# Kernel tuning notes

Measured on AMD Instinct MI355X. Metric: run time of the kernel, lower is better.

The kernel has to match this reference:

```python
import jax, jax.numpy as jnp
import numpy as np

B, CIN, COUT, L, K = 4, 512, 512, 4096, 7
DIL, STR = 1, 1
OUT_LEN = (L - DIL * (K - 1) - 1) // STR + 1  # 4090 ('valid' conv output length)


def setup_inputs() -> dict:
    key = jax.random.key(0)
    k1, k2, k3, k4 = jax.random.split(key, 4)
    x = jax.random.normal(k1, (B, CIN, L), dtype=jnp.float32)
    offsets = jax.random.normal(k2, (B, 1, OUT_LEN, K), dtype=jnp.float32)
    # kaiming_uniform_(a=sqrt(5)) on [COUT, CIN, K] -> U(-1/sqrt(fan_in), 1/sqrt(fan_in))
    fan_in = CIN * K
    bound = 1.0 / np.sqrt(fan_in)
    weight = jax.random.uniform(k3, (COUT, CIN, K), dtype=jnp.float32, minval=-bound, maxval=bound)
    bias = jax.random.uniform(k4, (COUT,), dtype=jnp.float32, minval=-bound, maxval=bound)
    return {"x": x, "offsets": offsets, "weight": weight, "bias": bias}


def _deform_interp(x, offsets, kernel_size, dilation, stride):
    # x: [B, C, L]; offsets: [B, 1, out_len, K] (offset_groups == 1)
    Lx = x.shape[-1]
    dil_pos = (jnp.arange(kernel_size) * dilation).astype(offsets.dtype)       # [K]
    out_len = offsets.shape[-2]
    t0s = (jnp.arange(out_len) * stride).astype(offsets.dtype)[:, None]        # [out_len, 1]
    T = t0s + dil_pos + offsets                                                # [B, 1, out_len, K]
    # constrained: each sample must stay inside its receptive field
    T = jnp.maximum(T, t0s)
    T = jnp.minimum(T, t0s + dil_pos[-1])
    U0 = jnp.clip(jnp.floor(T).astype(jnp.int32), 0, Lx - 2)                   # [B, 1, out_len, K]
    U = jnp.stack([U0, U0 + 1], axis=-1)                                       # [B, 1, out_len, K, 2]
    idx = U[:, 0]                                                              # [B, out_len, K, 2]
    # gather along length, broadcast index over channels
    xg = jax.vmap(lambda xb, ib: xb[:, ib])(x, idx)                            # [B, C, out_len, K, 2]
    # linear-interp weights: max(0, 1 - |U - T|)
    G = jnp.maximum(0.0, 1.0 - jnp.abs(U.astype(T.dtype) - T[..., None]))      # [B, 1, out_len, K, 2]
    return jnp.sum(G * xg, axis=-1)                                            # [B, C, out_len, K]


def reference(x, offsets, weight, bias):
    samp = _deform_interp(x, offsets, K, DIL, STR)                             # [B, C, out_len, K]
    # conv1d(weight, stride=K) on flattened [B, C, out_len*K] == per-position full contraction
    out = jnp.einsum('bcok,dck->bdo', samp, weight) + bias[:, None]            # [B, COUT, out_len]
    return out
```

## Files before the change

### kernel.cpp

```cpp
#include <hip/hip_runtime.h>
#include <hip/hip_bf16.h>
#include <stdint.h>

#define B_      4
#define CIN     512
#define COUT    512
#define L_      4096
#define K_      7
#define OUT_LEN 4090

typedef unsigned short ushort_t;
typedef __attribute__((ext_vector_type(8))) __bf16 bf16x8;
typedef __attribute__((ext_vector_type(4))) float f32x4;

__device__ __forceinline__ uint32_t f2bf(float f) {
    uint32_t u = __float_as_uint(f);
    return (u + 0x7fffu + ((u >> 16) & 1u)) >> 16;
}

__device__ __forceinline__ uint32_t pack2bf(float s0, float s1) {
    __hip_bfloat162 h = __float22bfloat162_rn(make_float2(s0, s1));
    uint32_t r;
    __builtin_memcpy(&r, &h, 4);
    return r;
}

__device__ __forceinline__ uint32_t interp1(uint32_t wl, uint32_t wh, float g0, float g1) {
    const float l0 = __uint_as_float(wl << 16);
    const float l1 = __uint_as_float(wl & 0xffff0000u);
    const float h0 = __uint_as_float(wh << 16);
    const float h1 = __uint_as_float(wh & 0xffff0000u);
    return pack2bf(g0 * l0 + g1 * h0, g0 * l1 + g1 * h1);
}

__device__ __forceinline__ void async16(const void* g, void* l) {
    __builtin_amdgcn_global_load_lds(
        (const __attribute__((address_space(1))) unsigned int*)g,
        (__attribute__((address_space(3))) unsigned int*)l, 16, 0, 0);
}


__global__ __launch_bounds__(256)
void reorder_w2_kernel(const float* __restrict__ w, uint32_t* __restrict__ Wr) {
    const int d   = blockIdx.x;
    const int tid = threadIdx.x;
    __shared__ float wrow[3584];
    const float4* src = (const float4*)(w + (size_t)d * 3584);
    for (int e = tid; e < 896; e += 256) ((float4*)wrow)[e] = src[e];
    __syncthreads();
    const int cc  = tid >> 4;
    const int clp = tid & 15;
    const int pos = (((clp >> 2) ^ ((d >> 1) & 3)) << 2) | (clp & 3);
    #pragma unroll
    for (int k = 0; k < K_; ++k) {
        const float w0 = wrow[tid * 14 + k];
        const float w1 = wrow[tid * 14 + 7 + k];
        Wr[((size_t)(cc * 7 + k) * 512 + d) * 16 + pos] = (f2bf(w1) << 16) | f2bf(w0);
    }
}

__global__ __launch_bounds__(256)
void interp_pack_kernel(const float* __restrict__ x, const float* __restrict__ offs,
                        uint32_t* __restrict__ P) {
    const int obx = blockIdx.x;
    const int cc  = blockIdx.y;
    const int b   = blockIdx.z;
    const int tid = threadIdx.x;
    const int o0  = obx * 128;
    __shared__ __align__(16) uint32_t XT[2176];

    const float* xc = x + ((size_t)b * CIN + cc * 32) * L_ + o0;
    #pragma unroll
    for (int r = 0; r < 3; ++r) {
        const int e = r * 256 + tid;
        if (e < 544) {
            const int cp   = e / 34;
            const int col4 = e - cp * 34;
            const int colb = col4 * 4;
            const float* p0 = xc + (size_t)(2 * cp) * L_ + colb;
            const float* p1 = p0 + L_;
            float4 v0, v1;
            if (o0 + colb + 3 < L_) {
                v0 = *(const float4*)p0;
                v1 = *(const float4*)p1;
            } else {
                float a0 = (o0 + colb + 0 < L_) ? p0[0] : 0.f;
                float a1 = (o0 + colb + 1 < L_) ? p0[1] : 0.f;
                float a2 = (o0 + colb + 2 < L_) ? p0[2] : 0.f;
                float a3 = (o0 + colb + 3 < L_) ? p0[3] : 0.f;
                float b0 = (o0 + colb + 0 < L_) ? p1[0] : 0.f;
                float b1 = (o0 + colb + 1 < L_) ? p1[1] : 0.f;
                float b2 = (o0 + colb + 2 < L_) ? p1[2] : 0.f;
                float b3 = (o0 + colb + 3 < L_) ? p1[3] : 0.f;
                v0 = make_float4(a0, a1, a2, a3);
                v1 = make_float4(b0, b1, b2, b3);
            }
            const float* f0 = (const float*)&v0;
            const float* f1 = (const float*)&v1;
            const int cpg = cp >> 1, hh = cp & 1;
            #pragma unroll
            for (int ii = 0; ii < 4; ++ii) {
                const int col = colb + ii;
                XT[col * 16 + (((cpg ^ (col & 7)) << 1) | hh)] = pack2bf(f0[ii], f1[ii]);
            }
        }
    }
    __syncthreads();

    const int o_loc = tid >> 1;
    const int h     = tid & 1;
    int o = o0 + o_loc; if (o > OUT_LEN - 1) o = OUT_LEN - 1;
    const float t0f = (float)o;
    const int sr = (o_loc >> 1) & 3;
    uint32_t* Pb = P + ((size_t)((b * 16 + cc) * 7) * 32 + obx) * 2048 + o_loc * 16;
    const int c0 = ((2 * h) ^ sr) << 2;
    const int c1 = ((2 * h + 1) ^ sr) << 2;
    #pragma unroll
    for (int k = 0; k < K_; ++k) {
        const float off = offs[((size_t)b * OUT_LEN + o) * K_ + k];
        float T = t0f + (float)k + off;
        T = fmaxf(T, t0f);
        T = fminf(T, t0f + 6.0f);
        int u0 = (int)floorf(T); if (u0 > L_ - 2) u0 = L_ - 2;
        const float g1 = T - (float)u0;
        const float g0 = 1.0f - g1;
        const int ul = u0 - o0;
        const uint32_t* R0 = &XT[ul * 16];
        const uint32_t* R1 = &XT[(ul + 1) * 16];
        const int s0 = ul & 7, s1 = (ul + 1) & 7;
        uint32_t ow[8];
        #pragma unroll
        for (int q = 0; q < 4; ++q) {
            const int pg = h * 4 + q;
            const uint2 lo = *(const uint2*)&R0[(pg ^ s0) << 1];
            const uint2 hi = *(const uint2*)&R1[(pg ^ s1) << 1];
            ow[q * 2 + 0] = interp1(lo.x, hi.x, g0, g1);
            ow[q * 2 + 1] = interp1(lo.y, hi.y, g0, g1);
        }
        uint32_t* Pk = Pb + (size_t)k * 65536;
        *(uint4*)&Pk[c0] = make_uint4(ow[0], ow[1], ow[2], ow[3]);
        *(uint4*)&Pk[c1] = make_uint4(ow[4], ow[5], ow[6], ow[7]);
    }
}

__global__ __launch_bounds__(256, 2)
void gemm_kernel(const ushort_t* __restrict__ Wr, const uint32_t* __restrict__ P,
                 const float* __restrict__ bias, float* __restrict__ out) {
    const int bxi  = blockIdx.x;
    const int o0   = bxi * 128;
    const int d0   = blockIdx.y * 128;
    const int b    = blockIdx.z;
    const int tid  = threadIdx.x;
    const int wv   = tid >> 6;
    const int lane = tid & 63;
    const int m16  = lane & 15;
    const int quad = lane >> 4;
    const int wd   = wv >> 1;
    const int wo   = wv & 1;
    const int sw   = (m16 >> 1) & 3;
    const int chk  = (quad ^ sw) * 8;

    __shared__ __align__(16) ushort_t As0[4096], As1[4096], As2[4096], As3[4096];
    __shared__ __align__(16) ushort_t Bs0[4096], Bs1[4096], Bs2[4096], Bs3[4096];

    const int aoff = (wd * 64 + m16) * 32 + chk;
    const int boff = (wo * 64 + m16) * 32 + chk;

    const ushort_t* Ag = Wr + (size_t)d0 * 32 + (size_t)tid * 8;
    const uint32_t* Bg = P + ((size_t)(b * 112) * 32 + bxi) * 2048 + (size_t)tid * 4;

#define ISSUE(S, ASP, BSP)                                                    \
    { _Pragma("unroll") for (int r_ = 0; r_ < 2; ++r_)                        \
        async16(Ag + (size_t)(S) * 16384 + r_ * 2048,                         \
                (void*)((ASP) + (r_ * 256 + wv * 64) * 8));                   \
      _Pragma("unroll") for (int r_ = 0; r_ < 2; ++r_)                        \
        async16(Bg + (size_t)(S) * 65536 + r_ * 1024,                         \
                (void*)((BSP) + (r_ * 256 + wv * 64) * 8)); }

#define WAITBAR(N)                                                            \
    { asm volatile("s_waitcnt vmcnt(" #N ")" ::: "memory");                   \
      __builtin_amdgcn_s_barrier();                                           \
      __builtin_amdgcn_sched_barrier(0); }

#define SSTEP(ASP, BSP)                                                       \
    {                                                                         \
        bf16x8 af_[4], bf_[4];                                                \
        _Pragma("unroll")                                                     \
        for (int i_ = 0; i_ < 4; ++i_) af_[i_] = *(const bf16x8*)&(ASP)[aoff + i_ * 512]; \
        _Pragma("unroll")                                                     \
        for (int j_ = 0; j_ < 4; ++j_) bf_[j_] = *(const bf16x8*)&(BSP)[boff + j_ * 512]; \
        __builtin_amdgcn_s_setprio(1);                                        \
        _Pragma("unroll")                                                     \
        for (int i_ = 0; i_ < 4; ++i_) {                                      \
            _Pragma("unroll")                                                 \
            for (int j_ = 0; j_ < 4; ++j_)                                    \
                acc[i_][j_] = __builtin_amdgcn_mfma_f32_16x16x32_bf16(        \
                    af_[i_], bf_[j_], acc[i_][j_], 0, 0, 0);                  \
        }                                                                     \
        __builtin_amdgcn_s_setprio(0);                                        \
    }

    f32x4 acc[4][4];
    #pragma unroll
    for (int i = 0; i < 4; ++i) {
        #pragma unroll
        for (int j = 0; j < 4; ++j) acc[i][j] = (f32x4){0.f, 0.f, 0.f, 0.f};
    }

    ISSUE(0, As0, Bs0);
    ISSUE(1, As1, Bs1);

    #pragma unroll 1
    for (int t = 0; t < 108; t += 4) {
        ISSUE(t + 2, As2, Bs2); WAITBAR(8); SSTEP(As0, Bs0);
        ISSUE(t + 3, As3, Bs3); WAITBAR(8); SSTEP(As1, Bs1);
        ISSUE(t + 4, As0, Bs0); WAITBAR(8); SSTEP(As2, Bs2);
        ISSUE(t + 5, As1, Bs1); WAITBAR(8); SSTEP(As3, Bs3);
    }
    ISSUE(110, As2, Bs2); WAITBAR(8); SSTEP(As0, Bs0);
    ISSUE(111, As3, Bs3); WAITBAR(8); SSTEP(As1, Bs1);
    WAITBAR(4); SSTEP(As2, Bs2);
    WAITBAR(0); SSTEP(As3, Bs3);

    #pragma unroll
    for (int i = 0; i < 4; ++i) {
        const int dd = d0 + wd * 64 + i * 16 + quad * 4;
        float bv[4];
        #pragma unroll
        for (int r = 0; r < 4; ++r) bv[r] = bias[dd + r];
        #pragma unroll
        for (int j = 0; j < 4; ++j) {
            const int oo = o0 + wo * 64 + j * 16 + m16;
            if (oo < OUT_LEN) {
                float* op = out + (size_t)b * COUT * OUT_LEN + (size_t)dd * OUT_LEN + oo;
                #pragma unroll
                for (int r = 0; r < 4; ++r)
                    op[(size_t)r * OUT_LEN] = acc[i][j][r] + bv[r];
            }
        }
    }
#undef ISSUE
#undef WAITBAR
#undef SSTEP
}


__global__ __launch_bounds__(256)
void reorder_w1_kernel(const float* __restrict__ w, uint32_t* __restrict__ Wr) {
    const int d   = blockIdx.x;
    const int tid = threadIdx.x;
    __shared__ float wrow[3584];
    const float4* src = (const float4*)(w + (size_t)d * 3584);
    for (int e = tid; e < 896; e += 256) ((float4*)wrow)[e] = src[e];
    __syncthreads();
    const int cc  = tid >> 4;
    const int clp = tid & 15;
    #pragma unroll
    for (int k = 0; k < K_; ++k) {
        const float w0 = wrow[tid * 14 + k];
        const float w1 = wrow[tid * 14 + 7 + k];
        Wr[((size_t)((k * 16 + cc) * 512 + d)) * 16 + clp] = (f2bf(w1) << 16) | f2bf(w0);
    }
}

__global__ __launch_bounds__(256)
void prepack_kernel(const float* __restrict__ x, uint32_t* __restrict__ xpack) {
    const int obx = blockIdx.x;
    const int cc  = blockIdx.y;
    const int b   = blockIdx.z;
    const int tid = threadIdx.x;
    const int o0  = obx * 128;
    __shared__ __align__(16) uint32_t XT[2176];
    const float* xc = x + ((size_t)b * CIN + cc * 32) * L_ + o0;
    #pragma unroll
    for (int r = 0; r < 3; ++r) {
        const int e = r * 256 + tid;
        if (e < 544) {
            const int cp   = e / 34;
            const int col4 = e - cp * 34;
            const int colb = col4 * 4;
            const float* p0 = xc + (size_t)(2 * cp) * L_ + colb;
            const float* p1 = p0 + L_;
            float4 v0, v1;
            if (o0 + colb + 3 < L_) {
                v0 = *(const float4*)p0;
                v1 = *(const float4*)p1;
            } else {
                float a0 = (o0 + colb + 0 < L_) ? p0[0] : 0.f;
                float a1 = (o0 + colb + 1 < L_) ? p0[1] : 0.f;
                float a2 = (o0 + colb + 2 < L_) ? p0[2] : 0.f;
                float a3 = (o0 + colb + 3 < L_) ? p0[3] : 0.f;
                float b0 = (o0 + colb + 0 < L_) ? p1[0] : 0.f;
                float b1 = (o0 + colb + 1 < L_) ? p1[1] : 0.f;
                float b2 = (o0 + colb + 2 < L_) ? p1[2] : 0.f;
                float b3 = (o0 + colb + 3 < L_) ? p1[3] : 0.f;
                v0 = make_float4(a0, a1, a2, a3);
                v1 = make_float4(b0, b1, b2, b3);
            }
            const float* f0 = (const float*)&v0;
            const float* f1 = (const float*)&v1;
            const int cpg = cp >> 1, h = cp & 1;
            #pragma unroll
            for (int ii = 0; ii < 4; ++ii) {
                const int col = colb + ii;
                XT[col * 16 + (((cpg ^ (col & 7)) << 1) | h)] = pack2bf(f0[ii], f1[ii]);
            }
        }
    }
    __syncthreads();
    uint4* dst = (uint4*)xpack + (size_t)((b * 16 + cc) * 32 + obx) * 544;
    const uint4* s4 = (const uint4*)XT;
    #pragma unroll
    for (int r = 0; r < 3; ++r) {
        const int e = r * 256 + tid;
        if (e < 544) dst[e] = s4[e];
    }
}

__global__ __launch_bounds__(256, 2)
void fused_v1_kernel(const float* __restrict__ offs, const ushort_t* __restrict__ Wr,
                     const uint32_t* __restrict__ xpack, const float* __restrict__ bias,
                     float* __restrict__ out) {
    const int bxi  = blockIdx.x;
    const int o0   = bxi * 128;
    const int d0   = blockIdx.y * 128;
    const int b    = blockIdx.z;
    const int tid  = threadIdx.x;
    const int wv   = tid >> 6;
    const int lane = tid & 63;
    const int m16  = lane & 15;
    const int quad = lane >> 4;
    const int ob   = wv * 32;
    const int q2   = quad * 2;

    __shared__ __align__(16) ushort_t As0[4096], As1[4096], As2[4096], As3[4096];
    __shared__ __align__(16) uint32_t XTB0[2304], XTB1[2304];
    __shared__ int    SU[896];
    __shared__ float2 PG[896];

#define ISSUE_A(KK, CC, ASP)                                                      \
    {                                                                             \
        _Pragma("unroll")                                                         \
        for (int r_ = 0; r_ < 2; ++r_) {                                          \
            const int c_ = r_ * 256 + tid;                                        \
            const int row_ = c_ >> 2, pc_ = c_ & 3;                               \
            const ushort_t* g_ = Wr                                               \
                + ((size_t)(((KK) * 16 + (CC)) * 512 + d0 + row_)) * 32 + pc_ * 8;\
            async16(g_, (void*)((ASP) + (r_ * 256 + wv * 64) * 8));               \
        }                                                                         \
    }

#define ISSUE_XTB(CC, XP)                                                         \
    {                                                                             \
        const uint32_t* sp_ = xpack + ((size_t)((b * 16 + (CC)) * 32 + bxi)) * 2176; \
        _Pragma("unroll")                                                         \
        for (int r_ = 0; r_ < 3; ++r_) {                                          \
            const int cb_ = r_ * 256 + wv * 64;                                   \
            if (cb_ < 544) {                                                      \
                const int c_ = r_ * 256 + tid;                                    \
                async16((const void*)(sp_ + (size_t)c_ * 4),                      \
                        (void*)((XP) + (size_t)cb_ * 4));                         \
            }                                                                     \
        }                                                                         \
    }

#define STEP(KK, XP, ASP)                                                         \
    {                                                                             \
        bf16x8 af_[8];                                                            \
        _Pragma("unroll")                                                         \
        for (int i_ = 0; i_ < 8; ++i_)                                            \
            af_[i_] = *(const bf16x8*)&(ASP)[(i_ * 16 + m16) * 32 + quad * 8];    \
        bf16x8 bfr_[2];                                                           \
        _Pragma("unroll")                                                         \
        for (int j_ = 0; j_ < 2; ++j_) {                                          \
            const int row_ = ((KK) << 7) | (ob + j_ * 16 + m16);                  \
            const int u_ = SU[row_];                                              \
            const float2 g_ = PG[row_];                                           \
            const uint32_t* Xr0_ = &(XP)[u_ * 16];                                \
            const uint32_t* Xr1_ = Xr0_ + 16;                                     \
            const int s0_ = u_ & 7, s1_ = (u_ + 1) & 7;                           \
            const uint2 a0_ = *(const uint2*)&Xr0_[((q2     ^ s0_) << 1)];        \
            const uint2 a1_ = *(const uint2*)&Xr0_[(((q2+1) ^ s0_) << 1)];        \
            const uint2 c0_ = *(const uint2*)&Xr1_[((q2     ^ s1_) << 1)];        \
            const uint2 c1_ = *(const uint2*)&Xr1_[(((q2+1) ^ s1_) << 1)];        \
            uint4 rr_;                                                            \
            rr_.x = interp1(a0_.x, c0_.x, g_.x, g_.y);                            \
            rr_.y = interp1(a0_.y, c0_.y, g_.x, g_.y);                            \
            rr_.z = interp1(a1_.x, c1_.x, g_.x, g_.y);                            \
            rr_.w = interp1(a1_.y, c1_.y, g_.x, g_.y);                            \
            __builtin_memcpy(&bfr_[j_], &rr_, 16);                                \
        }                                                                         \
        _Pragma("unroll")                                                         \
        for (int i_ = 0; i_ < 8; ++i_) {                                          \
            _Pragma("unroll")                                                     \
            for (int j_ = 0; j_ < 2; ++j_)                                        \
                acc[i_][j_] = __builtin_amdgcn_mfma_f32_16x16x32_bf16(af_[i_], bfr_[j_], acc[i_][j_], 0, 0, 0); \
        }                                                                         \
    }

#define HALF(CCB, A0_, A1_, A2_, A3_)                                             \
    ISSUE_A(2, (CCB), A2_); ISSUE_A(3, (CCB), A3_); ISSUE_XTB((CCB) + 1, XTB1);   \
    STEP(0, XTB0, A0_); STEP(1, XTB0, A1_); __syncthreads();                      \
    ISSUE_A(4, (CCB), A0_); ISSUE_A(5, (CCB), A1_);                               \
    STEP(2, XTB0, A2_); STEP(3, XTB0, A3_); __syncthreads();                      \
    ISSUE_A(6, (CCB), A2_); ISSUE_A(0, (CCB) + 1, A3_);                           \
    STEP(4, XTB0, A0_); STEP(5, XTB0, A1_); __syncthreads();                      \
    ISSUE_A(1, (CCB) + 1, A0_); ISSUE_A(2, (CCB) + 1, A1_);                       \
    STEP(6, XTB0, A2_); STEP(0, XTB1, A3_); __syncthreads();                      \
    ISSUE_A(3, (CCB) + 1, A2_); ISSUE_A(4, (CCB) + 1, A3_);                       \
    if ((CCB) + 2 < 16) { ISSUE_XTB((CCB) + 2, XTB0); }                           \
    STEP(1, XTB1, A0_); STEP(2, XTB1, A1_); __syncthreads();                      \
    ISSUE_A(5, (CCB) + 1, A0_); ISSUE_A(6, (CCB) + 1, A1_);                       \
    STEP(3, XTB1, A2_); STEP(4, XTB1, A3_); __syncthreads();                      \
    if ((CCB) + 2 < 16) { ISSUE_A(0, (CCB) + 2, A2_); ISSUE_A(1, (CCB) + 2, A3_); } \
    STEP(5, XTB1, A0_); STEP(6, XTB1, A1_); __syncthreads();

    f32x4 acc[8][2];
    #pragma unroll
    for (int i = 0; i < 8; ++i) {
        #pragma unroll
        for (int j = 0; j < 2; ++j) acc[i][j] = (f32x4){0.f, 0.f, 0.f, 0.f};
    }

    ISSUE_XTB(0, XTB0);
    ISSUE_A(0, 0, As0);
    ISSUE_A(1, 0, As1);
    for (int e = tid; e < 896; e += 256) {
        const int k  = e >> 7;
        const int ol = e & 127;
        int o = o0 + ol; if (o > OUT_LEN - 1) o = OUT_LEN - 1;
        const float t0  = (float)o;
        const float off = offs[((size_t)b * OUT_LEN + o) * K_ + k];
        float T = t0 + (float)k + off;
        T = fmaxf(T, t0);
        T = fminf(T, t0 + 6.0f);
        int u0 = (int)floorf(T);
        if (u0 > L_ - 2) u0 = L_ - 2;
        const float g0 = fmaxf(1.0f - fabsf((float)u0 - T), 0.0f);
        const float g1 = fmaxf(1.0f - fabsf((float)(u0 + 1) - T), 0.0f);
        SU[e] = u0 - o0;
        PG[e] = make_float2(g0, g1);
    }
    __syncthreads();

    #pragma unroll 1
    for (int s4 = 0; s4 < 16; s4 += 4) {
        HALF(s4,     As0, As1, As2, As3)
        HALF(s4 + 2, As2, As3, As0, As1)
    }

    #pragma unroll
    for (int i = 0; i < 8; ++i) {
        const int dd = d0 + i * 16 + quad * 4;
        float bv[4];
        #pragma unroll
        for (int r = 0; r < 4; ++r) bv[r] = bias[dd + r];
        #pragma unroll
        for (int j = 0; j < 2; ++j) {
            const int oo = o0 + ob + j * 16 + m16;
            if (oo < OUT_LEN) {
                float* op = out + (size_t)b * COUT * OUT_LEN + (size_t)dd * OUT_LEN + oo;
                #pragma unroll
                for (int r = 0; r < 4; ++r)
                    op[(size_t)r * OUT_LEN] = acc[i][j][r] + bv[r];
            }
        }
    }
#undef ISSUE_A
#undef ISSUE_XTB
#undef STEP
#undef HALF
}

#define BM 64
#define BN 64
#define BC 8
#define TT (BC * K_)

__global__ __launch_bounds__(256, 2)
void deform_conv1d_fallback(const float* __restrict__ x, const float* __restrict__ offsets,
                            const float* __restrict__ weight, const float* __restrict__ bias,
                            float* __restrict__ out) {
    const int o0 = blockIdx.x * BN, d0 = blockIdx.y * BM, b = blockIdx.z, tid = threadIdx.x;
    __shared__ int   SU[BN * K_];
    __shared__ float SG0[BN * K_], SG1[BN * K_];
    __shared__ float XT[BC][BN + 8];
    __shared__ float S[BC][K_][BN];
    __shared__ float WT[BM][TT + 1];
    for (int e = tid; e < BN * K_; e += 256) {
        const int ol = e / K_, k = e % K_, o = o0 + ol;
        int u0rel = 0; float g0 = 0.f, g1 = 0.f;
        if (o < OUT_LEN) {
            const float t0 = (float)o;
            const float off = offsets[(size_t)b * OUT_LEN * K_ + (size_t)o * K_ + k];
            float T = fminf(fmaxf(t0 + (float)k + off, t0), t0 + 6.0f);
            int u0 = (int)floorf(T); if (u0 > L_ - 2) u0 = L_ - 2;
            g0 = fmaxf(1.0f - fabsf((float)u0 - T), 0.0f);
            g1 = fmaxf(1.0f - fabsf((float)(u0 + 1) - T), 0.0f);
            u0rel = u0 - o0;
        }
        SU[e] = u0rel; SG0[e] = g0; SG1[e] = g1;
    }
    float acc[4][4];
    #pragma unroll
    for (int i = 0; i < 4; ++i) {
        #pragma unroll
        for (int j = 0; j < 4; ++j) acc[i][j] = 0.f;
    }
    const int ty = tid >> 4, tx = tid & 15;
    const float* xb = x + (size_t)b * CIN * L_;
    for (int c0 = 0; c0 < CIN; c0 += BC) {
        __syncthreads();
        for (int e = tid; e < BC * (BN + 7); e += 256) {
            const int cl = e / (BN + 7), j = e % (BN + 7), pos = o0 + j;
            XT[cl][j] = (pos < L_) ? xb[(size_t)(c0 + cl) * L_ + pos] : 0.f;
        }
        for (int e = tid; e < BM * TT; e += 256) {
            const int d = e / TT, t = e % TT;
            WT[d][t] = weight[(size_t)(d0 + d) * (CIN * K_) + c0 * K_ + t];
        }
        __syncthreads();
        for (int e = tid; e < BC * K_ * BN; e += 256) {
            const int cl = e / (K_ * BN), r = e % (K_ * BN), k = r / BN, ol = r % BN;
            const int p = ol * K_ + k, u = SU[p];
            S[cl][k][ol] = SG0[p] * XT[cl][u] + SG1[p] * XT[cl][u + 1];
        }
        __syncthreads();
        #pragma unroll
        for (int t = 0; t < TT; ++t) {
            const int cl = t / K_, k = t % K_;
            const float4 s4 = *(const float4*)&S[cl][k][tx * 4];
            const float w0 = WT[ty * 4 + 0][t], w1 = WT[ty * 4 + 1][t];
            const float w2 = WT[ty * 4 + 2][t], w3 = WT[ty * 4 + 3][t];
            acc[0][0] += w0 * s4.x; acc[0][1] += w0 * s4.y; acc[0][2] += w0 * s4.z; acc[0][3] += w0 * s4.w;
            acc[1][0] += w1 * s4.x; acc[1][1] += w1 * s4.y; acc[1][2] += w1 * s4.z; acc[1][3] += w1 * s4.w;
            acc[2][0] += w2 * s4.x; acc[2][1] += w2 * s4.y; acc[2][2] += w2 * s4.z; acc[2][3] += w2 * s4.w;
            acc[3][0] += w3 * s4.x; acc[3][1] += w3 * s4.y; acc[3][2] += w3 * s4.z; acc[3][3] += w3 * s4.w;
        }
    }
    #pragma unroll
    for (int i = 0; i < 4; ++i) {
        const int d = d0 + ty * 4 + i;
        const float bvv = bias[d];
        #pragma unroll
        for (int j = 0; j < 4; ++j) {
            const int o = o0 + tx * 4 + j;
            if (o < OUT_LEN)
                out[(size_t)b * COUT * OUT_LEN + (size_t)d * OUT_LEN + o] = acc[i][j] + bvv;
        }
    }
}

extern "C" void kernel_launch(void* const* d_in, const int* in_sizes, int n_in,
                              void* d_out, int out_size, void* d_ws, size_t ws_size,
                              hipStream_t stream) {
    const float* x       = (const float*)d_in[0];
    const float* offsets = (const float*)d_in[1];
    const float* weight  = (const float*)d_in[2];
    const float* bias    = (const float*)d_in[3];
    float* out = (float*)d_out;

    const size_t WR_BYTES = (size_t)512 * 512 * 7 * 2;
    const size_t P_BYTES  = (size_t)4 * 16 * 7 * 32 * 8192;
    const size_t XP_BYTES = (size_t)2048 * 544 * 16 + 512;

    if (ws_size >= WR_BYTES + P_BYTES) {
        uint32_t* Wr_u32 = (uint32_t*)d_ws;
        ushort_t* Wr     = (ushort_t*)d_ws;
        uint32_t* P      = (uint32_t*)((char*)d_ws + WR_BYTES);
        reorder_w2_kernel<<<512, 256, 0, stream>>>(weight, Wr_u32);
        interp_pack_kernel<<<dim3(32, 16, B_), 256, 0, stream>>>(x, offsets, P);
        gemm_kernel<<<dim3(32, 4, B_), 256, 0, stream>>>(Wr, P, bias, out);
        return;
    }

    if (ws_size >= WR_BYTES + XP_BYTES) {
        uint32_t* Wr_u32 = (uint32_t*)d_ws;
        ushort_t* Wr     = (ushort_t*)d_ws;
        uint32_t* xpack  = (uint32_t*)((char*)d_ws + WR_BYTES);
        reorder_w1_kernel<<<512, 256, 0, stream>>>(weight, Wr_u32);
        prepack_kernel<<<dim3(32, 16, B_), 256, 0, stream>>>(x, xpack);
        fused_v1_kernel<<<dim3(32, 4, B_), 256, 0, stream>>>(offsets, Wr, xpack, bias, out);
        return;
    }

    dim3 grid((OUT_LEN + BN - 1) / BN, COUT / BM, B_);
    deform_conv1d_fallback<<<grid, 256, 0, stream>>>(x, offsets, weight, bias, out);
}
```

Measured before the change: 169.1 us.

## Load GEMM weight fragments directly from global into registers, bypassing LDS

In the GEMM kernel the A-operand (reordered weights) no longer goes through four LDS stage buffers. Each wave now loads its bf16x8 fragments straight from global memory into four register stages, two steps ahead of use, and the vmcnt waits are raised to cover the extra loads. This halves the shared memory footprint and removes the LDS reads for A. In exchange it costs many more VGPRs (four register stages of A fragments), which may limit occupancy under the 2-block launch bound. Weight rows are also re-fetched from global or L2 by every wave instead of being shared through LDS.

```diff
diff --git a/kernel.cpp b/kernel.cpp
--- a/kernel.cpp
+++ b/kernel.cpp
@@ -160,33 +160,32 @@
     const int sw   = (m16 >> 1) & 3;
     const int chk  = (quad ^ sw) * 8;
 
-    __shared__ __align__(16) ushort_t As0[4096], As1[4096], As2[4096], As3[4096];
     __shared__ __align__(16) ushort_t Bs0[4096], Bs1[4096], Bs2[4096], Bs3[4096];
 
-    const int aoff = (wd * 64 + m16) * 32 + chk;
     const int boff = (wo * 64 + m16) * 32 + chk;
 
-    const ushort_t* Ag = Wr + (size_t)d0 * 32 + (size_t)tid * 8;
+    const ushort_t* Ab = Wr + (size_t)(d0 + wd * 64 + m16) * 32 + chk;
     const uint32_t* Bg = P + ((size_t)(b * 112) * 32 + bxi) * 2048 + (size_t)tid * 4;
 
-#define ISSUE(S, ASP, BSP)                                                    \
+#define DMAB(S, BSP)                                                          \
     { _Pragma("unroll") for (int r_ = 0; r_ < 2; ++r_)                        \
-        async16(Ag + (size_t)(S) * 16384 + r_ * 2048,                         \
-                (void*)((ASP) + (r_ * 256 + wv * 64) * 8));                   \
-      _Pragma("unroll") for (int r_ = 0; r_ < 2; ++r_)                        \
         async16(Bg + (size_t)(S) * 65536 + r_ * 1024,                         \
                 (void*)((BSP) + (r_ * 256 + wv * 64) * 8)); }
+
+#define LDA(AR, S)                                                            \
+    { const ushort_t* ap_ = Ab + (size_t)(S) * 16384;                         \
+      _Pragma("unroll")                                                       \
+      for (int i_ = 0; i_ < 4; ++i_)                                          \
+          AR[i_] = *(const bf16x8*)(ap_ + i_ * 512); }
 
 #define WAITBAR(N)                                                            \
     { asm volatile("s_waitcnt vmcnt(" #N ")" ::: "memory");                   \
       __builtin_amdgcn_s_barrier();                                           \
       __builtin_amdgcn_sched_barrier(0); }
 
-#define SSTEP(ASP, BSP)                                                       \
+#define SSTEP(BSP, AR)                                                        \
     {                                                                         \
-        bf16x8 af_[4], bf_[4];                                                \
-        _Pragma("unroll")                                                     \
-        for (int i_ = 0; i_ < 4; ++i_) af_[i_] = *(const bf16x8*)&(ASP)[aoff + i_ * 512]; \
+        bf16x8 bf_[4];                                                        \
         _Pragma("unroll")                                                     \
         for (int j_ = 0; j_ < 4; ++j_) bf_[j_] = *(const bf16x8*)&(BSP)[boff + j_ * 512]; \
         __builtin_amdgcn_s_setprio(1);                                        \
@@ -195,7 +194,7 @@
             _Pragma("unroll")                                                 \
             for (int j_ = 0; j_ < 4; ++j_)                                    \
                 acc[i_][j_] = __builtin_amdgcn_mfma_f32_16x16x32_bf16(        \
-                    af_[i_], bf_[j_], acc[i_][j_], 0, 0, 0);                  \
+                    AR[i_], bf_[j_], acc[i_][j_], 0, 0, 0);                   \
         }                                                                     \
         __builtin_amdgcn_s_setprio(0);                                        \
     }
@@ -207,20 +206,22 @@
         for (int j = 0; j < 4; ++j) acc[i][j] = (f32x4){0.f, 0.f, 0.f, 0.f};
     }
 
-    ISSUE(0, As0, Bs0);
-    ISSUE(1, As1, Bs1);
+    bf16x8 a0[4], a1[4], a2[4], a3[4];
+
+    DMAB(0, Bs0); LDA(a0, 0);
+    DMAB(1, Bs1); LDA(a1, 1);
 
     #pragma unroll 1
     for (int t = 0; t < 108; t += 4) {
-        ISSUE(t + 2, As2, Bs2); WAITBAR(8); SSTEP(As0, Bs0);
-        ISSUE(t + 3, As3, Bs3); WAITBAR(8); SSTEP(As1, Bs1);
-        ISSUE(t + 4, As0, Bs0); WAITBAR(8); SSTEP(As2, Bs2);
-        ISSUE(t + 5, As1, Bs1); WAITBAR(8); SSTEP(As3, Bs3);
-    }
-    ISSUE(110, As2, Bs2); WAITBAR(8); SSTEP(As0, Bs0);
-    ISSUE(111, As3, Bs3); WAITBAR(8); SSTEP(As1, Bs1);
-    WAITBAR(4); SSTEP(As2, Bs2);
-    WAITBAR(0); SSTEP(As3, Bs3);
+        DMAB(t + 2, Bs2); LDA(a2, t + 2); WAITBAR(12); SSTEP(Bs0, a0);
+        DMAB(t + 3, Bs3); LDA(a3, t + 3); WAITBAR(12); SSTEP(Bs1, a1);
+        DMAB(t + 4, Bs0); LDA(a0, t + 4); WAITBAR(12); SSTEP(Bs2, a2);
+        DMAB(t + 5, Bs1); LDA(a1, t + 5); WAITBAR(12); SSTEP(Bs3, a3);
+    }
+    DMAB(110, Bs2); LDA(a2, 110); WAITBAR(12); SSTEP(Bs0, a0);
+    DMAB(111, Bs3); LDA(a3, 111); WAITBAR(12); SSTEP(Bs1, a1);
+    WAITBAR(6);  SSTEP(Bs2, a2);
+    WAITBAR(0);  SSTEP(Bs3, a3);
 
     #pragma unroll
     for (int i = 0; i < 4; ++i) {
@@ -239,7 +240,8 @@
             }
         }
     }
-#undef ISSUE
+#undef DMAB
+#undef LDA
 #undef WAITBAR
 #undef SSTEP
 }
@@ -375,7 +377,7 @@
         for (int j_ = 0; j_ < 2; ++j_) {                                          \
             const int row_ = ((KK) << 7) | (ob + j_ * 16 + m16);                  \
             const int u_ = SU[row_];                                              \
-            const float2 g_ = PG[row_];                                           \
+            const float2 g_ = PG[row_];                                          \
             const uint32_t* Xr0_ = &(XP)[u_ * 16];                                \
             const uint32_t* Xr1_ = Xr0_ + 16;                                     \
             const int s0_ = u_ & 7, s1_ = (u_ + 1) & 7;                           \
```

Result: no change. 171.7 us (+1.5%).
